# Kernel tuning notes

Measured on AMD Instinct MI355X. Metric: run time of the kernel, lower is better.

Reference implementation:

```python
import jax, jax.numpy as jnp
import numpy as np

NUM_HEADS = 16
NUM_KV_HEADS = 4
HEAD_DIM = 128
D_MODEL = 2048


def setup_inputs() -> dict:
    key = jax.random.key(0)
    ks = jax.random.split(key, 6)
    B, S, d = 2, 2048, D_MODEL
    s_in = 1.0 / np.sqrt(d)
    return {
        "inputs_q": jax.random.normal(ks[0], (B, S, d), jnp.float32),
        "wq": jax.random.normal(ks[1], (d, NUM_HEADS * HEAD_DIM), jnp.float32) * s_in,
        "bq": jnp.zeros((NUM_HEADS * HEAD_DIM,), jnp.float32),
        "wk": jax.random.normal(ks[2], (d, NUM_KV_HEADS * HEAD_DIM), jnp.float32) * s_in,
        "bk": jnp.zeros((NUM_KV_HEADS * HEAD_DIM,), jnp.float32),
        "wv": jax.random.normal(ks[3], (d, NUM_KV_HEADS * HEAD_DIM), jnp.float32) * s_in,
        "bv": jnp.zeros((NUM_KV_HEADS * HEAD_DIM,), jnp.float32),
        "wo": jax.random.normal(ks[4], (NUM_HEADS * HEAD_DIM, d), jnp.float32) * s_in,
        "bo": jnp.zeros((d,), jnp.float32),
    }


def reference(inputs_q, wq, bq, wk, bk, wv, bv, wo, bo):
    B, S, _ = inputs_q.shape
    H, Hk, D = NUM_HEADS, NUM_KV_HEADS, HEAD_DIM
    G = H // Hk  # num_key_value_groups
    og_dtype = inputs_q.dtype

    # QKV projections (self-attention: inputs_kv is None)
    xq = (inputs_q @ wq + bq).reshape(B, S, H, D)
    xk = (inputs_q @ wk + bk).reshape(B, S, Hk, D)
    xv = (inputs_q @ wv + bv).reshape(B, S, Hk, D)

    # float32_attention upcast
    xq = xq.astype(jnp.float32)
    xk = xk.astype(jnp.float32)

    # GQA: q grouped as [B,S,Hk,G,D]; equivalent to repeat_interleave of k/v
    scale = 1.0 / np.sqrt(D)
    qg = (xq * scale).reshape(B, S, Hk, G, D)
    # attn_weights: [B, Hk, G, q, k]
    attn = jnp.einsum('bqhgd,bkhd->bhgqk', qg, xk)
    attn = jax.nn.softmax(attn.astype(jnp.float32), axis=-1).astype(xq.dtype)
    # dropout_p = 0.0 -> no-op
    out = jnp.einsum('bhgqk,bkhd->bqhgd', attn.astype(xv.dtype), xv)
    out = out.astype(og_dtype).reshape(B, S, H * D)
    return out @ wo + bo
```

## Files before the change

kernel.cpp:

```cpp
#include <hip/hip_runtime.h>


typedef __attribute__((ext_vector_type(4))) float f32x4;
typedef __attribute__((ext_vector_type(8))) short s16x8;
typedef __attribute__((ext_vector_type(4))) short s16x4;

__device__ __forceinline__ short f2bf(float f) {
  unsigned u = __builtin_bit_cast(unsigned, f);
  u += 0x7fffu + ((u >> 16) & 1u);
  return (short)(u >> 16);
}

__device__ __forceinline__ f32x4 mfma_bf16_16x16x32(s16x8 a, s16x8 b, f32x4 c) {
  asm("v_mfma_f32_16x16x32_bf16 %0, %1, %2, %0" : "+v"(c) : "v"(a), "v"(b));
  return c;
}

__device__ __forceinline__ void gload_lds16(const void* g, void* l) {
  __builtin_amdgcn_global_load_lds(
      (const __attribute__((address_space(1))) unsigned*)g,
      (__attribute__((address_space(3))) unsigned*)l, 16, 0, 0);
}

__global__ void k_cast(const float* __restrict__ in, short* __restrict__ out, int n4) {
  int i = blockIdx.x * blockDim.x + threadIdx.x;
  int stride = gridDim.x * blockDim.x;
  const f32x4* in4 = (const f32x4*)in;
  s16x4* out4 = (s16x4*)out;
  for (; i < n4; i += stride) {
    f32x4 v = in4[i];
    s16x4 o;
    o.x = f2bf(v.x); o.y = f2bf(v.y); o.z = f2bf(v.z); o.w = f2bf(v.w);
    out4[i] = o;
  }
}

__global__ void k_transpose_cast(const float* __restrict__ in, short* __restrict__ out,
                                 int R, int C) {
  __shared__ float t[32][33];
  int tx = threadIdx.x, ty = threadIdx.y;
  int c0 = blockIdx.x * 32, r0 = blockIdx.y * 32;
#pragma unroll
  for (int i = 0; i < 4; ++i)
    t[ty + 8 * i][tx] = in[(size_t)(r0 + ty + 8 * i) * C + (c0 + tx)];
  __syncthreads();
#pragma unroll
  for (int i = 0; i < 4; ++i)
    out[(size_t)(c0 + ty + 8 * i) * R + (r0 + tx)] = f2bf(t[tx][ty + 8 * i]);
}

__global__ void k_transpose_v(const short* __restrict__ XQKV, short* __restrict__ Vt) {
  __shared__ short t[32][33];
  int tx = threadIdx.x, ty = threadIdx.y;
  int s0 = blockIdx.x * 32, d0 = blockIdx.y * 32;
  int bh = blockIdx.z, b = bh >> 2, hk = bh & 3;
  const short* src = XQKV + (size_t)b * 2048 * 3072 + 2560 + hk * 128;
  short* dst = Vt + (size_t)bh * 128 * 2048;
#pragma unroll
  for (int i = 0; i < 4; ++i)
    t[ty + 8 * i][tx] = src[(size_t)(s0 + ty + 8 * i) * 3072 + (d0 + tx)];
  __syncthreads();
#pragma unroll
  for (int i = 0; i < 4; ++i)
    dst[(size_t)(d0 + ty + 8 * i) * 2048 + (s0 + tx)] = t[tx][ty + 8 * i];
}

__global__ void k_prep_k(const short* __restrict__ XQKV, short* __restrict__ Kc) {
  int cid = blockIdx.x * 256 + threadIdx.x;
  int l = cid & 63, ks = (cid >> 6) & 3, T = (cid >> 8) & 127, bh = cid >> 15;
  int ql = l & 15, g = l >> 4;
  int b = bh >> 2, hk = bh & 3;
  int s = T * 16 + ql;
  const s16x8 v = *(const s16x8*)(XQKV + ((size_t)b * 2048 + s) * 3072 + 2048 +
                                  hk * 128 + ks * 32 + g * 8);
  *(s16x8*)(Kc + (size_t)cid * 8) = v;
}

__global__ void k_prep_v(const short* __restrict__ Vt, short* __restrict__ Vc) {
  int cid = blockIdx.x * 256 + threadIdx.x;
  int l = cid & 63, dt = (cid >> 6) & 7, kvs = (cid >> 9) & 1;
  int U = (cid >> 10) & 31, bh = cid >> 15;
  int ql = l & 15, g = l >> 4;
  int dd = dt * 16 + ql, col = U * 64 + kvs * 32 + g * 8;
  const s16x8 v = *(const s16x8*)(Vt + (size_t)bh * 128 * 2048 + (size_t)dd * 2048 + col);
  *(s16x8*)(Vc + (size_t)cid * 8) = v;
}

template <int MODE>
__global__ __launch_bounds__(256) void k_gemm(const short* __restrict__ A,
                                              const short* __restrict__ Bt,
                                              const float* __restrict__ b0,
                                              const float* __restrict__ b1,
                                              const float* __restrict__ b2,
                                              void* __restrict__ Cout,
                                              int M, int N, int K) {
  __shared__ __align__(16) short lA[128 * 64];
  __shared__ __align__(16) short lB[128 * 64];
  const int tid = threadIdx.x;
  const int l = tid & 63, w = tid >> 6;
  const int ql = l & 15, g = l >> 4;
  const int wm = w >> 1, wn = w & 1;
  const int m0 = blockIdx.y * 128, n0 = blockIdx.x * 128;
  const int sr = l >> 3, sc = l & 7;

  f32x4 acc[4][4];
#pragma unroll
  for (int ii = 0; ii < 4; ++ii)
#pragma unroll
    for (int jj = 0; jj < 4; ++jj) acc[ii][jj] = (f32x4){0.f, 0.f, 0.f, 0.f};

  const int ktiles = K >> 6;
  for (int kt = 0; kt < ktiles; ++kt) {
    __syncthreads();
#pragma unroll
    for (int i = 0; i < 4; ++i) {
      int r = w * 32 + i * 8 + sr;
      int cg = sc ^ (r & 7);
      gload_lds16(A + (size_t)(m0 + r) * K + kt * 64 + cg * 8,
                  &lA[(w * 32 + i * 8) * 64]);
    }
#pragma unroll
    for (int i = 0; i < 4; ++i) {
      int r = w * 32 + i * 8 + sr;
      int cg = sc ^ (r & 7);
      gload_lds16(Bt + (size_t)(n0 + r) * K + kt * 64 + cg * 8,
                  &lB[(w * 32 + i * 8) * 64]);
    }
    __syncthreads();
#pragma unroll
    for (int ks = 0; ks < 2; ++ks) {
      s16x8 af[4], bf[4];
#pragma unroll
      for (int mi = 0; mi < 4; ++mi) {
        int r = wm * 64 + mi * 16 + ql;
        int ch = (ks * 4 + g) ^ (r & 7);
        af[mi] = *(const s16x8*)&lA[r * 64 + ch * 8];
      }
#pragma unroll
      for (int ni = 0; ni < 4; ++ni) {
        int r = wn * 64 + ni * 16 + ql;
        int ch = (ks * 4 + g) ^ (r & 7);
        bf[ni] = *(const s16x8*)&lB[r * 64 + ch * 8];
      }
#pragma unroll
      for (int mi = 0; mi < 4; ++mi)
#pragma unroll
        for (int ni = 0; ni < 4; ++ni)
          acc[mi][ni] = mfma_bf16_16x16x32(af[mi], bf[ni], acc[mi][ni]);
    }
  }

#pragma unroll
  for (int mi = 0; mi < 4; ++mi) {
#pragma unroll
    for (int ni = 0; ni < 4; ++ni) {
      int col = n0 + wn * 64 + ni * 16 + ql;
      int row0 = m0 + wm * 64 + mi * 16 + g * 4;
      float bias;
      if (MODE == 0)
        bias = (col < 2048) ? b0[col] : (col < 2560 ? b1[col - 2048] : b2[col - 2560]);
      else
        bias = b0[col];
      f32x4 v = acc[mi][ni];
      if (MODE == 0) {
        short* C = (short*)Cout;
#pragma unroll
        for (int j = 0; j < 4; ++j) C[(size_t)(row0 + j) * N + col] = f2bf(v[j] + bias);
      } else {
        float* C = (float*)Cout;
#pragma unroll
        for (int j = 0; j < 4; ++j) C[(size_t)(row0 + j) * N + col] = v[j] + bias;
      }
    }
  }
}

__global__ __launch_bounds__(512, 4) void k_attn(const short* __restrict__ XQKV,
                                                 const short* __restrict__ Kc,
                                                 const short* __restrict__ Vc,
                                                 short* __restrict__ Out) {
  __shared__ __align__(16) char smem[16384 + 16384 + 8 * 2304];
  short* lK = (short*)smem;
  short* lV = (short*)(smem + 16384);
  const int tid = threadIdx.x;
  const int l = tid & 63, w = tid >> 6;
  const int ql = l & 15, g = l >> 4;

  const int LID = blockIdx.x;
  const int grp = LID & 7;
  const int j = LID >> 3;
  const int b = grp >> 2, hk = grp & 3;
  const int h = hk * 4 + (j >> 4);
  const int bx = j & 15;
  const int bh = b * 4 + hk;

  const int q0 = bx * 128 + w * 16;
  const short* qp = XQKV + (size_t)b * 2048 * 3072 + h * 128;
  const short* kcb = Kc + (size_t)bh * 512 * 512;
  const short* vcb = Vc + (size_t)bh * 512 * 512;
  short(*P)[72] = (short(*)[72])(smem + 32768 + w * 2304);
  short* OLb = (short*)(smem + w * 4608);

  s16x8 qreg[4];
#pragma unroll
  for (int ks = 0; ks < 4; ++ks)
    qreg[ks] = *(const s16x8*)(qp + (size_t)(q0 + ql) * 3072 + ks * 32 + g * 8);

  float mo[4], ls[4];
#pragma unroll
  for (int jj = 0; jj < 4; ++jj) { mo[jj] = -1e30f; ls[jj] = 0.f; }
  f32x4 ot[8];
#pragma unroll
  for (int dt = 0; dt < 8; ++dt) ot[dt] = (f32x4){0.f, 0.f, 0.f, 0.f};

  const float scale = 0.08838834764831845f;

  for (int kt = 0; kt < 32; ++kt) {
    __syncthreads();
#pragma unroll
    for (int i = 0; i < 2; ++i) {
      int s = w * 2 + i;
      gload_lds16(kcb + ((size_t)kt * 16 + s) * 512 + l * 8, (char*)lK + s * 1024);
      gload_lds16(vcb + ((size_t)kt * 16 + s) * 512 + l * 8, (char*)lV + s * 1024);
    }
    __syncthreads();

    s16x8 kf[16];
#pragma unroll
    for (int f = 0; f < 16; ++f)
      kf[f] = *(const s16x8*)(lK + f * 512 + l * 8);

    f32x4 st[4];
#pragma unroll
    for (int t = 0; t < 4; ++t) st[t] = (f32x4){0.f, 0.f, 0.f, 0.f};
#pragma unroll
    for (int t = 0; t < 4; ++t)
#pragma unroll
      for (int ks = 0; ks < 4; ++ks)
        st[t] = mfma_bf16_16x16x32(qreg[ks], kf[t * 4 + ks], st[t]);

    float fac[4];
#pragma unroll
    for (int jj = 0; jj < 4; ++jj) {
#pragma unroll
      for (int t = 0; t < 4; ++t) st[t][jj] *= scale;
      float mt = fmaxf(fmaxf(st[0][jj], st[1][jj]), fmaxf(st[2][jj], st[3][jj]));
      mt = fmaxf(mt, __shfl_xor(mt, 1));
      mt = fmaxf(mt, __shfl_xor(mt, 2));
      mt = fmaxf(mt, __shfl_xor(mt, 4));
      mt = fmaxf(mt, __shfl_xor(mt, 8));
      float mn = fmaxf(mo[jj], mt);
      fac[jj] = __expf(mo[jj] - mn);
      mo[jj] = mn;
#pragma unroll
      for (int t = 0; t < 4; ++t) st[t][jj] = __expf(st[t][jj] - mn);
      float rs = st[0][jj] + st[1][jj] + st[2][jj] + st[3][jj];
      rs += __shfl_xor(rs, 1);
      rs += __shfl_xor(rs, 2);
      rs += __shfl_xor(rs, 4);
      rs += __shfl_xor(rs, 8);
      ls[jj] = ls[jj] * fac[jj] + rs;
    }

#pragma unroll
    for (int t = 0; t < 4; ++t)
#pragma unroll
      for (int jj = 0; jj < 4; ++jj)
        P[g * 4 + jj][t * 16 + ql] = f2bf(st[t][jj]);

    {
      int j2 = ql & 3;
      float fv = (j2 == 0) ? fac[0] : ((j2 == 1) ? fac[1] : ((j2 == 2) ? fac[2] : fac[3]));
      float facq = __shfl(fv, ((ql >> 2) << 4) | ql);
#pragma unroll
      for (int dt = 0; dt < 8; ++dt) {
        ot[dt][0] *= facq; ot[dt][1] *= facq; ot[dt][2] *= facq; ot[dt][3] *= facq;
      }
    }

    s16x8 vf[16];
#pragma unroll
    for (int f = 0; f < 16; ++f)
      vf[f] = *(const s16x8*)(lV + f * 512 + l * 8);
    s16x8 pf0 = *(const s16x8*)&P[ql][0 * 32 + g * 8];
    s16x8 pf1 = *(const s16x8*)&P[ql][1 * 32 + g * 8];
#pragma unroll
    for (int dt = 0; dt < 8; ++dt)
      ot[dt] = mfma_bf16_16x16x32(vf[dt], pf0, ot[dt]);
#pragma unroll
    for (int dt = 0; dt < 8; ++dt)
      ot[dt] = mfma_bf16_16x16x32(vf[8 + dt], pf1, ot[dt]);
  }

  __syncthreads();

  float iv[4];
#pragma unroll
  for (int jj = 0; jj < 4; ++jj) iv[jj] = 1.f / ls[jj];
  int j2 = ql & 3;
  float fv = (j2 == 0) ? iv[0] : ((j2 == 1) ? iv[1] : ((j2 == 2) ? iv[2] : iv[3]));
  float invq = __shfl(fv, ((ql >> 2) << 4) | ql);
#pragma unroll
  for (int dt = 0; dt < 8; ++dt)
#pragma unroll
    for (int jj = 0; jj < 4; ++jj)
      OLb[ql * 136 + dt * 16 + g * 4 + jj] = f2bf(ot[dt][jj] * invq);
#pragma unroll
  for (int pass = 0; pass < 4; ++pass) {
    int r = pass * 4 + g;
    s16x8 o = *(const s16x8*)&OLb[r * 136 + ql * 8];
    *(s16x8*)(Out + (size_t)(b * 2048 + q0 + r) * 2048 + h * 128 + ql * 8) = o;
  }
}

extern "C" void kernel_launch(void* const* d_in, const int* in_sizes, int n_in,
                              void* d_out, int out_size, void* d_ws, size_t ws_size,
                              hipStream_t stream) {
  const float* x  = (const float*)d_in[0];
  const float* wq = (const float*)d_in[1];
  const float* bq = (const float*)d_in[2];
  const float* wk = (const float*)d_in[3];
  const float* bk = (const float*)d_in[4];
  const float* wv = (const float*)d_in[5];
  const float* bv = (const float*)d_in[6];
  const float* wo = (const float*)d_in[7];
  const float* bo = (const float*)d_in[8];
  float* out = (float*)d_out;

  char* ws = (char*)d_ws;
  short* Xb   = (short*)(ws);
  short* Wqkv = (short*)(ws + (size_t)(16u << 20));
  short* Kc   = (short*)(ws + (size_t)(16u << 20));
  short* Vc   = (short*)(ws + (size_t)(20u << 20));
  short* WoT  = (short*)(ws + (size_t)(28u << 20));
  short* XQKV = (short*)(ws + (size_t)(36u << 20));
  short* Vt   = (short*)(ws + (size_t)(60u << 20));

  dim3 tb(32, 8);

  k_cast<<<2048, 256, 0, stream>>>(x, Xb, 4096 * 2048 / 4);
  k_transpose_cast<<<dim3(64, 64), tb, 0, stream>>>(wq, Wqkv, 2048, 2048);
  k_transpose_cast<<<dim3(16, 64), tb, 0, stream>>>(wk, Wqkv + (size_t)2048 * 2048, 2048, 512);
  k_transpose_cast<<<dim3(16, 64), tb, 0, stream>>>(wv, Wqkv + (size_t)2560 * 2048, 2048, 512);
  k_transpose_cast<<<dim3(64, 64), tb, 0, stream>>>(wo, WoT, 2048, 2048);

  k_gemm<0><<<dim3(3072 / 128, 4096 / 128), 256, 0, stream>>>(
      Xb, Wqkv, bq, bk, bv, (void*)XQKV, 4096, 3072, 2048);

  k_transpose_v<<<dim3(64, 4, 8), tb, 0, stream>>>(XQKV, Vt);
  k_prep_k<<<1024, 256, 0, stream>>>(XQKV, Kc);
  k_prep_v<<<1024, 256, 0, stream>>>(Vt, Vc);

  k_attn<<<dim3(512), 512, 0, stream>>>(XQKV, Kc, Vc, Xb);

  k_gemm<1><<<dim3(2048 / 128, 4096 / 128), 256, 0, stream>>>(
      Xb, WoT, bo, bo, bo, (void*)out, 4096, 2048, 2048);
}
```

Before: 255.3 us.

## Register-block attention waves over two query row groups to reuse K/V fragments

The attention kernel drops from 8 to 4 waves per block, and each wave now processes 32 query rows as two 16-row groups. Each K and V fragment read from shared memory feeds two MFMAs, one per row group, which halves LDS fragment traffic per unit of compute. Each wave also loads twice as many K/V rows from global memory into LDS. The trade-off is more accumulator and Q registers per wave and half as many resident waves per CU, which reduces latency hiding.

```diff
diff --git a/kernel.cpp b/kernel.cpp
--- a/kernel.cpp
+++ b/kernel.cpp
@@ -175,11 +175,11 @@
   }
 }
 
-__global__ __launch_bounds__(512, 4) void k_attn(const short* __restrict__ XQKV,
+__global__ __launch_bounds__(256, 2) void k_attn(const short* __restrict__ XQKV,
                                                  const short* __restrict__ Kc,
                                                  const short* __restrict__ Vc,
                                                  short* __restrict__ Out) {
-  __shared__ __align__(16) char smem[16384 + 16384 + 8 * 2304];
+  __shared__ __align__(16) char smem[16384 + 16384 + 4 * 4608];
   short* lK = (short*)smem;
   short* lV = (short*)(smem + 16384);
   const int tid = threadIdx.x;
@@ -194,122 +194,144 @@
   const int bx = j & 15;
   const int bh = b * 4 + hk;
 
-  const int q0 = bx * 128 + w * 16;
+  const int q0 = bx * 128 + w * 32;
   const short* qp = XQKV + (size_t)b * 2048 * 3072 + h * 128;
   const short* kcb = Kc + (size_t)bh * 512 * 512;
   const short* vcb = Vc + (size_t)bh * 512 * 512;
-  short(*P)[72] = (short(*)[72])(smem + 32768 + w * 2304);
+  short(*P)[72] = (short(*)[72])(smem + 32768 + w * 4608);
   short* OLb = (short*)(smem + w * 4608);
 
-  s16x8 qreg[4];
-#pragma unroll
-  for (int ks = 0; ks < 4; ++ks)
-    qreg[ks] = *(const s16x8*)(qp + (size_t)(q0 + ql) * 3072 + ks * 32 + g * 8);
-
-  float mo[4], ls[4];
-#pragma unroll
-  for (int jj = 0; jj < 4; ++jj) { mo[jj] = -1e30f; ls[jj] = 0.f; }
-  f32x4 ot[8];
-#pragma unroll
-  for (int dt = 0; dt < 8; ++dt) ot[dt] = (f32x4){0.f, 0.f, 0.f, 0.f};
+  s16x8 qreg[2][4];
+#pragma unroll
+  for (int rg = 0; rg < 2; ++rg)
+#pragma unroll
+    for (int ks = 0; ks < 4; ++ks)
+      qreg[rg][ks] =
+          *(const s16x8*)(qp + (size_t)(q0 + rg * 16 + ql) * 3072 + ks * 32 + g * 8);
+
+  float mo[2][4], ls[2][4];
+#pragma unroll
+  for (int rg = 0; rg < 2; ++rg)
+#pragma unroll
+    for (int jj = 0; jj < 4; ++jj) { mo[rg][jj] = -1e30f; ls[rg][jj] = 0.f; }
+  f32x4 ot[2][8];
+#pragma unroll
+  for (int rg = 0; rg < 2; ++rg)
+#pragma unroll
+    for (int dt = 0; dt < 8; ++dt) ot[rg][dt] = (f32x4){0.f, 0.f, 0.f, 0.f};
 
   const float scale = 0.08838834764831845f;
 
   for (int kt = 0; kt < 32; ++kt) {
     __syncthreads();
 #pragma unroll
-    for (int i = 0; i < 2; ++i) {
-      int s = w * 2 + i;
+    for (int i = 0; i < 4; ++i) {
+      int s = w * 4 + i;
       gload_lds16(kcb + ((size_t)kt * 16 + s) * 512 + l * 8, (char*)lK + s * 1024);
       gload_lds16(vcb + ((size_t)kt * 16 + s) * 512 + l * 8, (char*)lV + s * 1024);
     }
     __syncthreads();
 
-    s16x8 kf[16];
-#pragma unroll
-    for (int f = 0; f < 16; ++f)
-      kf[f] = *(const s16x8*)(lK + f * 512 + l * 8);
-
-    f32x4 st[4];
-#pragma unroll
-    for (int t = 0; t < 4; ++t) st[t] = (f32x4){0.f, 0.f, 0.f, 0.f};
+    f32x4 st[2][4];
+#pragma unroll
+    for (int rg = 0; rg < 2; ++rg)
+#pragma unroll
+      for (int t = 0; t < 4; ++t) st[rg][t] = (f32x4){0.f, 0.f, 0.f, 0.f};
 #pragma unroll
     for (int t = 0; t < 4; ++t)
 #pragma unroll
-      for (int ks = 0; ks < 4; ++ks)
-        st[t] = mfma_bf16_16x16x32(qreg[ks], kf[t * 4 + ks], st[t]);
-
-    float fac[4];
-#pragma unroll
-    for (int jj = 0; jj < 4; ++jj) {
-#pragma unroll
-      for (int t = 0; t < 4; ++t) st[t][jj] *= scale;
-      float mt = fmaxf(fmaxf(st[0][jj], st[1][jj]), fmaxf(st[2][jj], st[3][jj]));
-      mt = fmaxf(mt, __shfl_xor(mt, 1));
-      mt = fmaxf(mt, __shfl_xor(mt, 2));
-      mt = fmaxf(mt, __shfl_xor(mt, 4));
-      mt = fmaxf(mt, __shfl_xor(mt, 8));
-      float mn = fmaxf(mo[jj], mt);
-      fac[jj] = __expf(mo[jj] - mn);
-      mo[jj] = mn;
-#pragma unroll
-      for (int t = 0; t < 4; ++t) st[t][jj] = __expf(st[t][jj] - mn);
-      float rs = st[0][jj] + st[1][jj] + st[2][jj] + st[3][jj];
-      rs += __shfl_xor(rs, 1);
-      rs += __shfl_xor(rs, 2);
-      rs += __shfl_xor(rs, 4);
-      rs += __shfl_xor(rs, 8);
-      ls[jj] = ls[jj] * fac[jj] + rs;
-    }
-
-#pragma unroll
-    for (int t = 0; t < 4; ++t)
+      for (int ks = 0; ks < 4; ++ks) {
+        s16x8 kf = *(const s16x8*)(lK + (t * 4 + ks) * 512 + l * 8);
+        st[0][t] = mfma_bf16_16x16x32(qreg[0][ks], kf, st[0][t]);
+        st[1][t] = mfma_bf16_16x16x32(qreg[1][ks], kf, st[1][t]);
+      }
+
+    float fac[2][4];
+#pragma unroll
+    for (int rg = 0; rg < 2; ++rg)
+#pragma unroll
+      for (int jj = 0; jj < 4; ++jj) {
+#pragma unroll
+        for (int t = 0; t < 4; ++t) st[rg][t][jj] *= scale;
+        float mt = fmaxf(fmaxf(st[rg][0][jj], st[rg][1][jj]),
+                         fmaxf(st[rg][2][jj], st[rg][3][jj]));
+        mt = fmaxf(mt, __shfl_xor(mt, 1));
+        mt = fmaxf(mt, __shfl_xor(mt, 2));
+        mt = fmaxf(mt, __shfl_xor(mt, 4));
+        mt = fmaxf(mt, __shfl_xor(mt, 8));
+        float mn = fmaxf(mo[rg][jj], mt);
+        fac[rg][jj] = __expf(mo[rg][jj] - mn);
+        mo[rg][jj] = mn;
+#pragma unroll
+        for (int t = 0; t < 4; ++t) st[rg][t][jj] = __expf(st[rg][t][jj] - mn);
+        float rs = st[rg][0][jj] + st[rg][1][jj] + st[rg][2][jj] + st[rg][3][jj];
+        rs += __shfl_xor(rs, 1);
+        rs += __shfl_xor(rs, 2);
+        rs += __shfl_xor(rs, 4);
+        rs += __shfl_xor(rs, 8);
+        ls[rg][jj] = ls[rg][jj] * fac[rg][jj] + rs;
+      }
+
+#pragma unroll
+    for (int rg = 0; rg < 2; ++rg)
+#pragma unroll
+      for (int t = 0; t < 4; ++t)
+#pragma unroll
+        for (int jj = 0; jj < 4; ++jj)
+          P[rg * 16 + g * 4 + jj][t * 16 + ql] = f2bf(st[rg][t][jj]);
+
+#pragma unroll
+    for (int rg = 0; rg < 2; ++rg) {
+      int j2 = ql & 3;
+      float fv = (j2 == 0) ? fac[rg][0]
+               : ((j2 == 1) ? fac[rg][1] : ((j2 == 2) ? fac[rg][2] : fac[rg][3]));
+      float facq = __shfl(fv, ((ql >> 2) << 4) | ql);
+#pragma unroll
+      for (int dt = 0; dt < 8; ++dt) {
+        ot[rg][dt][0] *= facq; ot[rg][dt][1] *= facq;
+        ot[rg][dt][2] *= facq; ot[rg][dt][3] *= facq;
+      }
+    }
+
+    s16x8 pf00 = *(const s16x8*)&P[ql][0 * 32 + g * 8];
+    s16x8 pf01 = *(const s16x8*)&P[ql][1 * 32 + g * 8];
+    s16x8 pf10 = *(const s16x8*)&P[16 + ql][0 * 32 + g * 8];
+    s16x8 pf11 = *(const s16x8*)&P[16 + ql][1 * 32 + g * 8];
+#pragma unroll
+    for (int dt = 0; dt < 8; ++dt) {
+      s16x8 vf = *(const s16x8*)(lV + dt * 512 + l * 8);
+      ot[0][dt] = mfma_bf16_16x16x32(vf, pf00, ot[0][dt]);
+      ot[1][dt] = mfma_bf16_16x16x32(vf, pf10, ot[1][dt]);
+    }
+#pragma unroll
+    for (int dt = 0; dt < 8; ++dt) {
+      s16x8 vf = *(const s16x8*)(lV + (8 + dt) * 512 + l * 8);
+      ot[0][dt] = mfma_bf16_16x16x32(vf, pf01, ot[0][dt]);
+      ot[1][dt] = mfma_bf16_16x16x32(vf, pf11, ot[1][dt]);
+    }
+  }
+
+  __syncthreads();
+
+#pragma unroll
+  for (int rg = 0; rg < 2; ++rg) {
+    float iv[4];
+#pragma unroll
+    for (int jj = 0; jj < 4; ++jj) iv[jj] = 1.f / ls[rg][jj];
+    int j2 = ql & 3;
+    float fv = (j2 == 0) ? iv[0] : ((j2 == 1) ? iv[1] : ((j2 == 2) ? iv[2] : iv[3]));
+    float invq = __shfl(fv, ((ql >> 2) << 4) | ql);
+#pragma unroll
+    for (int dt = 0; dt < 8; ++dt)
 #pragma unroll
       for (int jj = 0; jj < 4; ++jj)
-        P[g * 4 + jj][t * 16 + ql] = f2bf(st[t][jj]);
-
-    {
-      int j2 = ql & 3;
-      float fv = (j2 == 0) ? fac[0] : ((j2 == 1) ? fac[1] : ((j2 == 2) ? fac[2] : fac[3]));
-      float facq = __shfl(fv, ((ql >> 2) << 4) | ql);
-#pragma unroll
-      for (int dt = 0; dt < 8; ++dt) {
-        ot[dt][0] *= facq; ot[dt][1] *= facq; ot[dt][2] *= facq; ot[dt][3] *= facq;
-      }
-    }
-
-    s16x8 vf[16];
-#pragma unroll
-    for (int f = 0; f < 16; ++f)
-      vf[f] = *(const s16x8*)(lV + f * 512 + l * 8);
-    s16x8 pf0 = *(const s16x8*)&P[ql][0 * 32 + g * 8];
-    s16x8 pf1 = *(const s16x8*)&P[ql][1 * 32 + g * 8];
-#pragma unroll
-    for (int dt = 0; dt < 8; ++dt)
-      ot[dt] = mfma_bf16_16x16x32(vf[dt], pf0, ot[dt]);
-#pragma unroll
-    for (int dt = 0; dt < 8; ++dt)
-      ot[dt] = mfma_bf16_16x16x32(vf[8 + dt], pf1, ot[dt]);
-  }
-
-  __syncthreads();
-
-  float iv[4];
-#pragma unroll
-  for (int jj = 0; jj < 4; ++jj) iv[jj] = 1.f / ls[jj];
-  int j2 = ql & 3;
-  float fv = (j2 == 0) ? iv[0] : ((j2 == 1) ? iv[1] : ((j2 == 2) ? iv[2] : iv[3]));
-  float invq = __shfl(fv, ((ql >> 2) << 4) | ql);
-#pragma unroll
-  for (int dt = 0; dt < 8; ++dt)
-#pragma unroll
-    for (int jj = 0; jj < 4; ++jj)
-      OLb[ql * 136 + dt * 16 + g * 4 + jj] = f2bf(ot[dt][jj] * invq);
-#pragma unroll
-  for (int pass = 0; pass < 4; ++pass) {
-    int r = pass * 4 + g;
-    s16x8 o = *(const s16x8*)&OLb[r * 136 + ql * 8];
-    *(s16x8*)(Out + (size_t)(b * 2048 + q0 + r) * 2048 + h * 128 + ql * 8) = o;
+        OLb[ql * 136 + dt * 16 + g * 4 + jj] = f2bf(ot[rg][dt][jj] * invq);
+#pragma unroll
+    for (int pass = 0; pass < 4; ++pass) {
+      int r = pass * 4 + g;
+      s16x8 o = *(const s16x8*)&OLb[r * 136 + ql * 8];
+      *(s16x8*)(Out + (size_t)(b * 2048 + q0 + rg * 16 + r) * 2048 + h * 128 + ql * 8) = o;
+    }
   }
 }
 
@@ -351,7 +373,7 @@
   k_prep_k<<<1024, 256, 0, stream>>>(XQKV, Kc);
   k_prep_v<<<1024, 256, 0, stream>>>(Vt, Vc);
 
-  k_attn<<<dim3(512), 512, 0, stream>>>(XQKV, Kc, Vc, Xb);
+  k_attn<<<dim3(512), 256, 0, stream>>>(XQKV, Kc, Vc, Xb);
 
   k_gemm<1><<<dim3(2048 / 128, 4096 / 128), 256, 0, stream>>>(
       Xb, WoT, bo, bo, bo, (void*)out, 4096, 2048, 2048);
```

New measurement: 261.1 us. +2.2%, slower.

## Fuse K/V fragment-layout scatter into QKV GEMM epilogue, drop prep kernels

Applied to the files above, without the earlier changes.

The QKV projection GEMM epilogue now writes Q into a dedicated contiguous buffer and scatters K and V directly into the MFMA fragment layouts the attention kernel consumes. This removes three separate kernels (V transpose, K prep, V prep) and the extra global round trips they made. The cost is scattered 2-byte stores in the GEMM epilogue, which may coalesce poorly. Workspace offsets are reorganized to match.

```diff
diff --git a/kernel.cpp b/kernel.cpp
--- a/kernel.cpp
+++ b/kernel.cpp
@@ -49,43 +49,6 @@
     out[(size_t)(c0 + ty + 8 * i) * R + (r0 + tx)] = f2bf(t[tx][ty + 8 * i]);
 }
 
-__global__ void k_transpose_v(const short* __restrict__ XQKV, short* __restrict__ Vt) {
-  __shared__ short t[32][33];
-  int tx = threadIdx.x, ty = threadIdx.y;
-  int s0 = blockIdx.x * 32, d0 = blockIdx.y * 32;
-  int bh = blockIdx.z, b = bh >> 2, hk = bh & 3;
-  const short* src = XQKV + (size_t)b * 2048 * 3072 + 2560 + hk * 128;
-  short* dst = Vt + (size_t)bh * 128 * 2048;
-#pragma unroll
-  for (int i = 0; i < 4; ++i)
-    t[ty + 8 * i][tx] = src[(size_t)(s0 + ty + 8 * i) * 3072 + (d0 + tx)];
-  __syncthreads();
-#pragma unroll
-  for (int i = 0; i < 4; ++i)
-    dst[(size_t)(d0 + ty + 8 * i) * 2048 + (s0 + tx)] = t[tx][ty + 8 * i];
-}
-
-__global__ void k_prep_k(const short* __restrict__ XQKV, short* __restrict__ Kc) {
-  int cid = blockIdx.x * 256 + threadIdx.x;
-  int l = cid & 63, ks = (cid >> 6) & 3, T = (cid >> 8) & 127, bh = cid >> 15;
-  int ql = l & 15, g = l >> 4;
-  int b = bh >> 2, hk = bh & 3;
-  int s = T * 16 + ql;
-  const s16x8 v = *(const s16x8*)(XQKV + ((size_t)b * 2048 + s) * 3072 + 2048 +
-                                  hk * 128 + ks * 32 + g * 8);
-  *(s16x8*)(Kc + (size_t)cid * 8) = v;
-}
-
-__global__ void k_prep_v(const short* __restrict__ Vt, short* __restrict__ Vc) {
-  int cid = blockIdx.x * 256 + threadIdx.x;
-  int l = cid & 63, dt = (cid >> 6) & 7, kvs = (cid >> 9) & 1;
-  int U = (cid >> 10) & 31, bh = cid >> 15;
-  int ql = l & 15, g = l >> 4;
-  int dd = dt * 16 + ql, col = U * 64 + kvs * 32 + g * 8;
-  const s16x8 v = *(const s16x8*)(Vt + (size_t)bh * 128 * 2048 + (size_t)dd * 2048 + col);
-  *(s16x8*)(Vc + (size_t)cid * 8) = v;
-}
-
 template <int MODE>
 __global__ __launch_bounds__(256) void k_gemm(const short* __restrict__ A,
                                               const short* __restrict__ Bt,
@@ -93,6 +56,8 @@
                                               const float* __restrict__ b1,
                                               const float* __restrict__ b2,
                                               void* __restrict__ Cout,
+                                              short* __restrict__ Kc,
+                                              short* __restrict__ Vc,
                                               int M, int N, int K) {
   __shared__ __align__(16) short lA[128 * 64];
   __shared__ __align__(16) short lB[128 * 64];
@@ -163,9 +128,33 @@
         bias = b0[col];
       f32x4 v = acc[mi][ni];
       if (MODE == 0) {
-        short* C = (short*)Cout;
-#pragma unroll
-        for (int j = 0; j < 4; ++j) C[(size_t)(row0 + j) * N + col] = f2bf(v[j] + bias);
+        if (col < 2048) {
+          short* Qb = (short*)Cout;
+#pragma unroll
+          for (int j = 0; j < 4; ++j)
+            Qb[(size_t)(row0 + j) * 2048 + col] = f2bf(v[j] + bias);
+        } else if (col < 2560) {
+          int c = col - 2048, hk = c >> 7, d = c & 127;
+          int ks2 = d >> 5, g2 = (d >> 3) & 3, pos = d & 7;
+#pragma unroll
+          for (int j = 0; j < 4; ++j) {
+            int row = row0 + j, b2 = row >> 11, s = row & 2047;
+            int T = s >> 4, lane = (s & 15) + 16 * g2;
+            size_t idx = ((((size_t)(b2 * 4 + hk) * 128 + T) * 4 + ks2) * 64 + lane) * 8 + pos;
+            Kc[idx] = f2bf(v[j] + bias);
+          }
+        } else {
+          int c = col - 2560, hk = c >> 7, dd = c & 127;
+          int dt2 = dd >> 4, ql2 = dd & 15;
+#pragma unroll
+          for (int j = 0; j < 4; ++j) {
+            int row = row0 + j, b2 = row >> 11, s = row & 2047;
+            int U = s >> 6, kvs = (s >> 5) & 1, g2 = (s >> 3) & 3, pos = s & 7;
+            int lane = ql2 + 16 * g2;
+            size_t idx = (((((size_t)(b2 * 4 + hk) * 32 + U) * 2 + kvs) * 8 + dt2) * 64 + lane) * 8 + pos;
+            Vc[idx] = f2bf(v[j] + bias);
+          }
+        }
       } else {
         float* C = (float*)Cout;
 #pragma unroll
@@ -175,7 +164,7 @@
   }
 }
 
-__global__ __launch_bounds__(512, 4) void k_attn(const short* __restrict__ XQKV,
+__global__ __launch_bounds__(512, 4) void k_attn(const short* __restrict__ Qb,
                                                  const short* __restrict__ Kc,
                                                  const short* __restrict__ Vc,
                                                  short* __restrict__ Out) {
@@ -195,7 +184,7 @@
   const int bh = b * 4 + hk;
 
   const int q0 = bx * 128 + w * 16;
-  const short* qp = XQKV + (size_t)b * 2048 * 3072 + h * 128;
+  const short* qp = Qb + (size_t)b * 2048 * 2048 + h * 128;
   const short* kcb = Kc + (size_t)bh * 512 * 512;
   const short* vcb = Vc + (size_t)bh * 512 * 512;
   short(*P)[72] = (short(*)[72])(smem + 32768 + w * 2304);
@@ -204,7 +193,7 @@
   s16x8 qreg[4];
 #pragma unroll
   for (int ks = 0; ks < 4; ++ks)
-    qreg[ks] = *(const s16x8*)(qp + (size_t)(q0 + ql) * 3072 + ks * 32 + g * 8);
+    qreg[ks] = *(const s16x8*)(qp + (size_t)(q0 + ql) * 2048 + ks * 32 + g * 8);
 
   float mo[4], ls[4];
 #pragma unroll
@@ -330,11 +319,10 @@
   char* ws = (char*)d_ws;
   short* Xb   = (short*)(ws);
   short* Wqkv = (short*)(ws + (size_t)(16u << 20));
-  short* Kc   = (short*)(ws + (size_t)(16u << 20));
-  short* Vc   = (short*)(ws + (size_t)(20u << 20));
   short* WoT  = (short*)(ws + (size_t)(28u << 20));
-  short* XQKV = (short*)(ws + (size_t)(36u << 20));
-  short* Vt   = (short*)(ws + (size_t)(60u << 20));
+  short* Qb   = (short*)(ws + (size_t)(36u << 20));
+  short* Kc   = (short*)(ws + (size_t)(52u << 20));
+  short* Vc   = (short*)(ws + (size_t)(56u << 20));
 
   dim3 tb(32, 8);
 
@@ -345,14 +333,10 @@
   k_transpose_cast<<<dim3(64, 64), tb, 0, stream>>>(wo, WoT, 2048, 2048);
 
   k_gemm<0><<<dim3(3072 / 128, 4096 / 128), 256, 0, stream>>>(
-      Xb, Wqkv, bq, bk, bv, (void*)XQKV, 4096, 3072, 2048);
-
-  k_transpose_v<<<dim3(64, 4, 8), tb, 0, stream>>>(XQKV, Vt);
-  k_prep_k<<<1024, 256, 0, stream>>>(XQKV, Kc);
-  k_prep_v<<<1024, 256, 0, stream>>>(Vt, Vc);
-
-  k_attn<<<dim3(512), 512, 0, stream>>>(XQKV, Kc, Vc, Xb);
+      Xb, Wqkv, bq, bk, bv, (void*)Qb, Kc, Vc, 4096, 3072, 2048);
+
+  k_attn<<<dim3(512), 512, 0, stream>>>(Qb, Kc, Vc, Xb);
 
   k_gemm<1><<<dim3(2048 / 128, 4096 / 128), 256, 0, stream>>>(
-      Xb, WoT, bo, bo, bo, (void*)out, 4096, 2048, 2048);
-}
+      Xb, WoT, bo, bo, bo, (void*)out, nullptr, nullptr, 4096, 2048, 2048);
+}
```

Result: faster. 247.4 us (-3.1%).
